# Kernel tuning notes

Measured on AMD Instinct MI355X. Metric: run time of the kernel, lower is better.

Reference implementation:

```python
import jax, jax.numpy as jnp
import numpy as np

R, B, F, H, C = 32, 2048, 512, 1024, 100  # n_rules, batch, n_fea, 2*n_fea, n_cls


def setup_inputs() -> dict:
    key = jax.random.key(0)
    ks = jax.random.split(key, 10)
    sc = lambda k, shape, fan: (jax.random.normal(k, shape, jnp.float32) / np.float32(np.sqrt(fan)))
    return {
        "data": jax.random.normal(ks[0], (B, F), jnp.float32),
        "proto": jax.random.normal(ks[1], (R, F), jnp.float32),
        "var": jax.random.uniform(ks[2], (R, F), jnp.float32, 0.5, 1.5),
        "fs_w1": sc(ks[3], (F, H), F), "fs_b1": jnp.zeros((H,), jnp.float32),
        "fs_w2": sc(ks[4], (H, F), H), "fs_b2": jnp.zeros((F,), jnp.float32),
        "fs_w3": sc(ks[5], (F, 1), F), "fs_b3": jnp.zeros((1,), jnp.float32),
        "cq_w1": sc(ks[6], (R, F, H), F), "cq_b1": jnp.zeros((R, H), jnp.float32),
        "cq_w2": sc(ks[7], (R, H, F), H), "cq_b2": jnp.zeros((R, F), jnp.float32),
        "cq_w3": sc(ks[8], (R, F, C), F), "cq_b3": jnp.zeros((R, C), jnp.float32),
        "is_train": 1,
    }


def reference(data, proto, var, fs_w1, fs_b1, fs_w2, fs_b2, fs_w3, fs_b3,
              cq_w1, cq_b1, cq_w2, cq_b2, cq_w3, cq_b3, is_train):
    # Gaussian fuzzy membership per rule: [R, B, F]
    fuzzy = jnp.exp(-(data[None, :, :] - proto[:, None, :]) ** 2
                    / (2.0 * var[:, None, :] ** 2))
    # shared fire-strength MLP applied per rule
    h = jax.nn.relu(jnp.einsum('rbf,fh->rbh', fuzzy, fs_w1) + fs_b1)
    h = jax.nn.relu(jnp.einsum('rbh,hf->rbf', h, fs_w2) + fs_b2)
    fs_logits = (jnp.einsum('rbf,fo->rbo', h, fs_w3) + fs_b3)[..., 0]  # [R, B]
    fire = jax.nn.softmax(fs_logits.T, axis=1)  # [B, R], softmax over rules
    # per-rule consequent MLPs on raw data (grouped GEMMs)
    g = jax.nn.relu(jnp.einsum('bf,rfh->rbh', data, cq_w1) + cq_b1[:, None, :])
    g = jax.nn.relu(jnp.einsum('rbh,rhf->rbf', g, cq_w2) + cq_b2[:, None, :])
    logits = jnp.einsum('rbf,rfc->rbc', g, cq_w3) + cq_b3[:, None, :]  # [R, B, C]
    # softmax-weighted expert sum, then class softmax
    out = jnp.einsum('br,rbc->bc', fire, logits)  # [B, C]
    return jax.nn.softmax(out, axis=1)
```

## Files before the change

kernel.cpp:

```cpp
#include <hip/hip_runtime.h>

typedef __attribute__((ext_vector_type(8))) short short8;
typedef __attribute__((ext_vector_type(4))) float f32x4;

__device__ __forceinline__ unsigned short f2bf(float f) {
    union { float f; unsigned u; } v; v.f = f;
    unsigned r = v.u + 0x7FFFu + ((v.u >> 16) & 1u);
    return (unsigned short)(r >> 16);
}
__device__ __forceinline__ float bf2f(unsigned short u) {
    union { unsigned u; float f; } v; v.u = ((unsigned)u) << 16;
    return v.f;
}

__global__ __launch_bounds__(256)
void cvt_bf16_kernel(const float* __restrict__ X, unsigned short* __restrict__ Y, int n4) {
    int i = blockIdx.x * 256 + threadIdx.x;
    if (i >= n4) return;
    float4 v = ((const float4*)X)[i];
    ushort4 o; o.x = f2bf(v.x); o.y = f2bf(v.y); o.z = f2bf(v.z); o.w = f2bf(v.w);
    ((ushort4*)Y)[i] = o;
}

__global__ __launch_bounds__(256)
void transpose_kernel(const float* __restrict__ X, unsigned short* __restrict__ Y,
                      int K, int N, int Np) {
    __shared__ float tile[32][33];
    int g = blockIdx.z;
    const float* Xg = X + (long)g * K * N;
    unsigned short* Yg = Y + (long)g * Np * K;
    int k0 = blockIdx.x * 32, n0 = blockIdx.y * 32;
    int tx = threadIdx.x & 31, ty = threadIdx.x >> 5;
#pragma unroll
    for (int i = 0; i < 4; ++i) {
        int kk = ty + i * 8;
        int n = n0 + tx;
        tile[kk][tx] = (n < N) ? Xg[(long)(k0 + kk) * N + n] : 0.0f;
    }
    __syncthreads();
#pragma unroll
    for (int i = 0; i < 4; ++i) {
        int nn = ty + i * 8;
        Yg[(long)(n0 + nn) * K + k0 + tx] = f2bf(tile[tx][nn]);
    }
}

__global__ __launch_bounds__(128)
void fuzzy_kernel(const float* __restrict__ data, const float* __restrict__ proto,
                  const float* __restrict__ var, unsigned short* __restrict__ fuzzy,
                  int r0) {
    int rb = blockIdx.x;
    int r = r0 + (rb >> 11), b = rb & 2047;
    int f = threadIdx.x * 4;
    float4 d = *(const float4*)(data + (long)b * 512 + f);
    float4 p = *(const float4*)(proto + (long)r * 512 + f);
    float4 w = *(const float4*)(var + (long)r * 512 + f);
    ushort4 o;
    float x;
    x = d.x - p.x; o.x = f2bf(__expf(-(x * x) / (2.f * w.x * w.x)));
    x = d.y - p.y; o.y = f2bf(__expf(-(x * x) / (2.f * w.y * w.y)));
    x = d.z - p.z; o.z = f2bf(__expf(-(x * x) / (2.f * w.z * w.z)));
    x = d.w - p.w; o.w = f2bf(__expf(-(x * x) / (2.f * w.w * w.w)));
    *(ushort4*)(fuzzy + (long)rb * 512 + f) = o;
}

#define RING_WAIT_BARRIER(n)                                        \
    asm volatile("s_waitcnt vmcnt(" #n ")" ::: "memory");           \
    __builtin_amdgcn_sched_barrier(0);                              \
    __builtin_amdgcn_s_barrier();                                   \
    __builtin_amdgcn_sched_barrier(0);

template<int EPI, bool RELU>
__global__ __launch_bounds__(512, 2)
void gemm256_kernel(const unsigned short* __restrict__ A,
                    const unsigned short* __restrict__ Bt,
                    const float* __restrict__ bias,
                    void* __restrict__ Cptr,
                    const float* __restrict__ w3,
                    float* __restrict__ fslog,
                    int nM, int nN, int K,
                    long sAg, long sBg, long sCg, int sBiasG) {
    unsigned tot = gridDim.x, bid = blockIdx.x;
    unsigned sw = (bid & 7u) * (tot >> 3) + (bid >> 3);
    unsigned pg = (unsigned)(nM * nN);
    unsigned g = sw / pg;
    unsigned rem = sw - g * pg;
    const int m0 = (int)(rem / (unsigned)nN) * 256;
    const int n0 = (int)(rem % (unsigned)nN) * 256;
    const int N = nN * 256;
    A += (long)g * sAg; Bt += (long)g * sBg; bias += (long)g * sBiasG;

    __shared__ __align__(16) unsigned short lds[8][8192];

    const int tid = threadIdx.x;
    const int lane = tid & 63;
    const int w = tid >> 6;
    const int wm = w >> 2, wn = w & 3;
    const int r16 = lane & 15, kg = lane >> 4;

    f32x4 acc[8][4];
#pragma unroll
    for (int i = 0; i < 8; ++i)
#pragma unroll
        for (int j = 0; j < 4; ++j) {
            f32x4 z = {0.f, 0.f, 0.f, 0.f};
            acc[i][j] = z;
        }

    const int nsteps = K >> 5;

    auto STAGE = [&](int slot, int kt) {
        const int k0 = kt << 5;
#pragma unroll
        for (int j = 0; j < 2; ++j) {
            int f = j * 512 + tid;
            int row = f >> 2, sl = f & 3;
            int kk = (sl ^ ((row >> 1) & 3)) << 3;
            const unsigned short* ga = A + (long)(m0 + row) * K + k0 + kk;
            __builtin_amdgcn_global_load_lds(
                (const __attribute__((address_space(1))) void*)ga,
                (__attribute__((address_space(3))) void*)(&lds[slot][0] + (j * 512 + w * 64) * 8),
                16, 0, 0);
            const unsigned short* gb = Bt + (long)(n0 + row) * K + k0 + kk;
            __builtin_amdgcn_global_load_lds(
                (const __attribute__((address_space(1))) void*)gb,
                (__attribute__((address_space(3))) void*)(&lds[4 + slot][0] + (j * 512 + w * 64) * 8),
                16, 0, 0);
        }
    };

    auto COMPUTE = [&](int slot) {
        short8 aF[8], bF[4];
#pragma unroll
        for (int mt = 0; mt < 8; ++mt) {
            int R = wm * 128 + mt * 16 + r16;
            aF[mt] = *(const short8*)(&lds[slot][0] + R * 32 + ((kg ^ ((R >> 1) & 3)) << 3));
        }
#pragma unroll
        for (int nt = 0; nt < 4; ++nt) {
            int R = wn * 64 + nt * 16 + r16;
            bF[nt] = *(const short8*)(&lds[4 + slot][0] + R * 32 + ((kg ^ ((R >> 1) & 3)) << 3));
        }
        __builtin_amdgcn_s_setprio(1);
#pragma unroll
        for (int mt = 0; mt < 8; ++mt)
#pragma unroll
            for (int nt = 0; nt < 4; ++nt)
                acc[mt][nt] = __builtin_amdgcn_mfma_f32_16x16x32_bf16(
                    aF[mt], bF[nt], acc[mt][nt], 0, 0, 0);
        __builtin_amdgcn_s_setprio(0);
        asm volatile("" ::: "memory");
        __builtin_amdgcn_s_barrier();
        __builtin_amdgcn_sched_barrier(0);
    };

    STAGE(0, 0); STAGE(1, 1); STAGE(2, 2);
    for (int t = 0; t <= nsteps - 3; ++t) {
        if (t + 3 < nsteps) STAGE((t + 3) & 3, t + 3);
        RING_WAIT_BARRIER(8);
        COMPUTE(t & 3);
    }
    { RING_WAIT_BARRIER(4); COMPUTE((nsteps - 2) & 3); }
    { RING_WAIT_BARRIER(0); COMPUTE((nsteps - 1) & 3); }

    if constexpr (EPI == 1) {
        float w3v[4], bv[4];
#pragma unroll
        for (int nt = 0; nt < 4; ++nt) {
            int col = n0 + wn * 64 + nt * 16 + r16;
            w3v[nt] = w3[col];
            bv[nt] = bias[col];
        }
#pragma unroll
        for (int mt = 0; mt < 8; ++mt) {
#pragma unroll
            for (int j = 0; j < 4; ++j) {
                float p = 0.f;
#pragma unroll
                for (int nt = 0; nt < 4; ++nt) {
                    float v = acc[mt][nt][j] + bv[nt];
                    if (RELU) v = fmaxf(v, 0.f);
                    p += v * w3v[nt];
                }
                p += __shfl_xor(p, 1, 64);
                p += __shfl_xor(p, 2, 64);
                p += __shfl_xor(p, 4, 64);
                p += __shfl_xor(p, 8, 64);
                if (r16 == 0) {
                    int row = m0 + wm * 128 + mt * 16 + kg * 4 + j;
                    atomicAdd(&fslog[row], p);
                }
            }
        }
    } else {
#pragma unroll
        for (int nt = 0; nt < 4; ++nt) {
            int col = n0 + wn * 64 + nt * 16 + r16;
            float bv = bias[col];
#pragma unroll
            for (int mt = 0; mt < 8; ++mt) {
#pragma unroll
                for (int j = 0; j < 4; ++j) {
                    int row = m0 + wm * 128 + mt * 16 + kg * 4 + j;
                    float v = acc[mt][nt][j] + bv;
                    if (RELU) v = fmaxf(v, 0.f);
                    ((unsigned short*)Cptr)[(long)g * sCg + (long)row * N + col] = f2bf(v);
                }
            }
        }
    }
}

template<int EPI, bool RELU>
__global__ __launch_bounds__(256, 2)
void gemm_kernel(const unsigned short* __restrict__ A,
                 const unsigned short* __restrict__ Bt,
                 const float* __restrict__ bias,
                 void* __restrict__ Cptr,
                 int nM, int nN, int K,
                 long sAg, long sBg, long sCg, int sBiasG, int biasN) {
    unsigned tot = gridDim.x;
    unsigned bid = blockIdx.x;
    unsigned sw = (tot & 7u) == 0 ? (bid & 7u) * (tot >> 3) + (bid >> 3) : bid;
    unsigned pg = (unsigned)nM * (unsigned)nN;
    unsigned g = sw / pg;
    unsigned rem = sw - g * pg;
    unsigned mt_ = rem / (unsigned)nN;
    unsigned nt_ = rem - mt_ * (unsigned)nN;
    const int N = nN * 128;
    A += (long)g * sAg;
    Bt += (long)g * sBg;
    bias += (long)g * sBiasG;
    const int m0 = (int)mt_ * 128;
    const int n0 = (int)nt_ * 128;

    __shared__ __align__(16) unsigned short ldsA[128 * 32];
    __shared__ __align__(16) unsigned short ldsB[128 * 32];

    const int tid = threadIdx.x;
    const int lane = tid & 63;
    const int w = tid >> 6;
    const int wm = w >> 1, wn = w & 1;
    const int r16 = lane & 15, kg = lane >> 4;

    f32x4 acc[4][4];
#pragma unroll
    for (int i = 0; i < 4; ++i)
#pragma unroll
        for (int j = 0; j < 4; ++j) {
            f32x4 z = {0.f, 0.f, 0.f, 0.f};
            acc[i][j] = z;
        }

    for (int k0 = 0; k0 < K; k0 += 32) {
#pragma unroll
        for (int j = 0; j < 2; ++j) {
            int t = j * 256 + tid;
            int row = t >> 2, kc = (t & 3) * 8;
            const unsigned short* ga = A + (long)(m0 + row) * K + k0 + kc;
            __builtin_amdgcn_global_load_lds(
                (const __attribute__((address_space(1))) void*)ga,
                (__attribute__((address_space(3))) void*)(ldsA + (j * 256 + w * 64) * 8),
                16, 0, 0);
            const unsigned short* gb = Bt + (long)(n0 + row) * K + k0 + kc;
            __builtin_amdgcn_global_load_lds(
                (const __attribute__((address_space(1))) void*)gb,
                (__attribute__((address_space(3))) void*)(ldsB + (j * 256 + w * 64) * 8),
                16, 0, 0);
        }
        __syncthreads();
        short8 aF[4], bF[4];
#pragma unroll
        for (int mt = 0; mt < 4; ++mt)
            aF[mt] = *(const short8*)(ldsA + (wm * 64 + mt * 16 + r16) * 32 + kg * 8);
#pragma unroll
        for (int nt = 0; nt < 4; ++nt)
            bF[nt] = *(const short8*)(ldsB + (wn * 64 + nt * 16 + r16) * 32 + kg * 8);
#pragma unroll
        for (int mt = 0; mt < 4; ++mt)
#pragma unroll
            for (int nt = 0; nt < 4; ++nt)
                acc[mt][nt] = __builtin_amdgcn_mfma_f32_16x16x32_bf16(
                    aF[mt], bF[nt], acc[mt][nt], 0, 0, 0);
        __syncthreads();
    }

#pragma unroll
    for (int nt = 0; nt < 4; ++nt) {
        int col = n0 + wn * 64 + nt * 16 + r16;
        float bv = (col < biasN) ? bias[col] : 0.f;
#pragma unroll
        for (int mt = 0; mt < 4; ++mt) {
#pragma unroll
            for (int j = 0; j < 4; ++j) {
                int row = m0 + wm * 64 + mt * 16 + kg * 4 + j;
                float v = acc[mt][nt][j] + bv;
                if (RELU) v = fmaxf(v, 0.f);
                if constexpr (EPI == 0)
                    ((unsigned short*)Cptr)[(long)g * sCg + (long)row * N + col] = f2bf(v);
                else
                    ((float*)Cptr)[(long)g * sCg + (long)row * N + col] = v;
            }
        }
    }
}

__global__ __launch_bounds__(256)
void fire_kernel(const float* __restrict__ fslog, float* __restrict__ fire) {
    int b = blockIdx.x * 256 + threadIdx.x;
    float v[32];
    float mx = -1e30f;
#pragma unroll
    for (int r = 0; r < 32; ++r) { v[r] = fslog[r * 2048 + b]; mx = fmaxf(mx, v[r]); }
    float s = 0.f;
#pragma unroll
    for (int r = 0; r < 32; ++r) { v[r] = __expf(v[r] - mx); s += v[r]; }
    float inv = 1.f / s;
#pragma unroll
    for (int r = 0; r < 32; ++r) fire[b * 32 + r] = v[r] * inv;
}

__global__ __launch_bounds__(128)
void accum_kernel(const float* __restrict__ logits, const float* __restrict__ fire,
                  float* __restrict__ mix, int r0, int NR, int first) {
    int b = blockIdx.x, c = threadIdx.x;
    float acc = first ? 0.f : mix[b * 128 + c];
    for (int r = 0; r < NR; ++r)
        acc += fire[b * 32 + r0 + r] * logits[((long)r * 2048 + b) * 128 + c];
    mix[b * 128 + c] = acc;
}

__global__ __launch_bounds__(128)
void softmax_out_kernel(const float* __restrict__ mix, float* __restrict__ out) {
    int b = blockIdx.x, c = threadIdx.x;
    __shared__ float redm[2], reds[2];
    float val = (c < 100) ? mix[b * 128 + c] : -1e30f;
    float m = val;
#pragma unroll
    for (int off = 32; off; off >>= 1) m = fmaxf(m, __shfl_xor(m, off, 64));
    int lane = c & 63, wv = c >> 6;
    if (lane == 0) redm[wv] = m;
    __syncthreads();
    m = fmaxf(redm[0], redm[1]);
    float e = (c < 100) ? __expf(val - m) : 0.f;
    float s = e;
#pragma unroll
    for (int off = 32; off; off >>= 1) s += __shfl_xor(s, off, 64);
    if (lane == 0) reds[wv] = s;
    __syncthreads();
    s = reds[0] + reds[1];
    if (c < 100) out[b * 100 + c] = e / s;
}

extern "C" void kernel_launch(void* const* d_in, const int* in_sizes, int n_in,
                              void* d_out, int out_size, void* d_ws, size_t ws_size,
                              hipStream_t stream) {
    const float* data  = (const float*)d_in[0];
    const float* proto = (const float*)d_in[1];
    const float* var   = (const float*)d_in[2];
    const float* fs_w1 = (const float*)d_in[3];
    const float* fs_b1 = (const float*)d_in[4];
    const float* fs_w2 = (const float*)d_in[5];
    const float* fs_b2 = (const float*)d_in[6];
    const float* fs_w3 = (const float*)d_in[7];
    const float* cq_w1 = (const float*)d_in[9];
    const float* cq_b1 = (const float*)d_in[10];
    const float* cq_w2 = (const float*)d_in[11];
    const float* cq_b2 = (const float*)d_in[12];
    const float* cq_w3 = (const float*)d_in[13];
    const float* cq_b3 = (const float*)d_in[14];
    float* out = (float*)d_out;

    const size_t PERSIST = 2097152 + 1048576 + 1048576 + 262144 + 262144 + 1048576;
    const size_t PER_RULE_P2 = 1048576 + 1048576 + 131072 + 2097152;
    auto need = [&](int p1r, int p2r) -> size_t {
        size_t logitsC = (size_t)p2r * 2048 * 128 * 4;
        size_t R0 = (size_t)p1r * 2048 * 512 * 2;
        size_t r0p2 = (size_t)p2r * PER_RULE_P2;
        if (r0p2 > R0) R0 = r0p2;
        size_t R1 = (size_t)p1r * 2048 * 1024 * 2;
        size_t g1b = (size_t)p2r * 2048 * 1024 * 2;
        if (g1b > R1) R1 = g1b;
        return PERSIST + logitsC + R0 + R1;
    };
    int p1r = 32, p2r = 16;
    while (need(p1r, p2r) > ws_size && p1r > 2) { p1r >>= 1; p2r >>= 1; }

    char* ws = (char*)d_ws;
    size_t off = 0;
    auto take = [&](size_t bytes) { char* p = ws + off; off += bytes; return p; };
    unsigned short* data_bf = (unsigned short*)take(2097152);
    unsigned short* w1t     = (unsigned short*)take(1048576);
    unsigned short* w2t     = (unsigned short*)take(1048576);
    float*          fslog   = (float*)take(262144);
    float*          fire    = (float*)take(262144);
    float*          mix     = (float*)take(1048576);
    float*          logitsC = (float*)take((size_t)p2r * 2048 * 128 * 4);
    size_t R0sz = (size_t)p1r * 2048 * 512 * 2;
    { size_t t = (size_t)p2r * PER_RULE_P2; if (t > R0sz) R0sz = t; }
    char* R0 = take(R0sz);
    size_t R1sz = (size_t)p1r * 2048 * 1024 * 2;
    { size_t t = (size_t)p2r * 2048 * 1024 * 2; if (t > R1sz) R1sz = t; }
    char* R1 = take(R1sz);

    unsigned short* cF   = (unsigned short*)R0;
    unsigned short* cW1t = (unsigned short*)R0;
    unsigned short* cW2t = (unsigned short*)(R0 + (size_t)p2r * 1048576);
    unsigned short* cW3t = (unsigned short*)(R0 + (size_t)p2r * 2097152);
    unsigned short* g2   = (unsigned short*)(R0 + (size_t)p2r * 2097152 + (size_t)p2r * 131072);
    unsigned short* h1   = (unsigned short*)R1;
    unsigned short* g1   = (unsigned short*)R1;

    cvt_bf16_kernel<<<1024, 256, 0, stream>>>(data, data_bf, 262144);
    transpose_kernel<<<dim3(16, 32, 1), 256, 0, stream>>>(fs_w1, w1t, 512, 1024, 1024);
    transpose_kernel<<<dim3(32, 16, 1), 256, 0, stream>>>(fs_w2, w2t, 1024, 512, 512);
    hipMemsetAsync(fslog, 0, 262144, stream);

    for (int ch = 0; ch < 32 / p1r; ++ch) {
        const int r0 = ch * p1r;
        fuzzy_kernel<<<p1r * 2048, 128, 0, stream>>>(data, proto, var, cF, r0);
        gemm256_kernel<0, true><<<p1r * 8 * 4, 512, 0, stream>>>(
            cF, w1t, fs_b1, h1, nullptr, nullptr,
            p1r * 8, 4, 512, 0, 0, 0, 0);
        gemm256_kernel<1, true><<<p1r * 8 * 2, 512, 0, stream>>>(
            h1, w2t, fs_b2, nullptr, fs_w3, fslog + (long)r0 * 2048,
            p1r * 8, 2, 1024, 0, 0, 0, 0);
    }
    fire_kernel<<<8, 256, 0, stream>>>(fslog, fire);

    for (int ch = 0; ch < 32 / p2r; ++ch) {
        const int r0 = ch * p2r;
        transpose_kernel<<<dim3(16, 32, p2r), 256, 0, stream>>>(
            cq_w1 + (long)r0 * 512 * 1024, cW1t, 512, 1024, 1024);
        transpose_kernel<<<dim3(32, 16, p2r), 256, 0, stream>>>(
            cq_w2 + (long)r0 * 1024 * 512, cW2t, 1024, 512, 512);
        transpose_kernel<<<dim3(16, 4, p2r), 256, 0, stream>>>(
            cq_w3 + (long)r0 * 512 * 100, cW3t, 512, 100, 128);
        gemm256_kernel<0, true><<<8 * 4 * p2r, 512, 0, stream>>>(
            data_bf, cW1t, cq_b1 + (long)r0 * 1024, g1, nullptr, nullptr,
            8, 4, 512, 0, (long)1024 * 512, (long)2048 * 1024, 1024);
        gemm256_kernel<0, true><<<8 * 2 * p2r, 512, 0, stream>>>(
            g1, cW2t, cq_b2 + (long)r0 * 512, g2, nullptr, nullptr,
            8, 2, 1024, (long)2048 * 1024, (long)512 * 1024, (long)2048 * 512, 512);
        gemm_kernel<2, false><<<16 * 1 * p2r, 256, 0, stream>>>(
            g2, cW3t, cq_b3 + (long)r0 * 100, logitsC,
            16, 1, 512, (long)2048 * 512, (long)128 * 512, (long)2048 * 128, 100, 100);
        accum_kernel<<<2048, 128, 0, stream>>>(logitsC, fire, mix, r0, p2r, ch == 0);
    }
    softmax_out_kernel<<<2048, 128, 0, stream>>>(mix, out);
}
```

Before: 536.7 us.

## Fuse fuzzy membership into first GEMM, fuse expert mixing into final GEMM

The Gaussian membership computation moves into the A-operand staging of a new first fire-strength GEMM, so the bf16 fuzzy tensor is never materialized. The reciprocal 1/(2·var²) is precomputed once. The per-rule logits GEMM now atomically accumulates fire-weighted outputs straight into the mix buffer, which removes the logits buffer and the accum kernel. The bf16 GEMM epilogue now stages through LDS to make 16-byte coalesced stores, and the rule chunking for phase one is removed by allocating the full h1 buffer. The costs are larger workspace, heavy float atomics on mix, and exp work sitting inside the GEMM main loop.

```diff
diff --git a/kernel.cpp b/kernel.cpp
--- a/kernel.cpp
+++ b/kernel.cpp
@@ -7,10 +7,6 @@
     union { float f; unsigned u; } v; v.f = f;
     unsigned r = v.u + 0x7FFFu + ((v.u >> 16) & 1u);
     return (unsigned short)(r >> 16);
-}
-__device__ __forceinline__ float bf2f(unsigned short u) {
-    union { unsigned u; float f; } v; v.u = ((unsigned)u) << 16;
-    return v.f;
 }
 
 __global__ __launch_bounds__(256)
@@ -20,6 +16,14 @@
     float4 v = ((const float4*)X)[i];
     ushort4 o; o.x = f2bf(v.x); o.y = f2bf(v.y); o.z = f2bf(v.z); o.w = f2bf(v.w);
     ((ushort4*)Y)[i] = o;
+}
+
+__global__ __launch_bounds__(256)
+void prep_var_kernel(const float* __restrict__ var, float* __restrict__ iv2, int n) {
+    int i = blockIdx.x * 256 + threadIdx.x;
+    if (i >= n) return;
+    float v = var[i];
+    iv2[i] = 1.f / (2.f * v * v);
 }
 
 __global__ __launch_bounds__(256)
@@ -43,25 +47,6 @@
         int nn = ty + i * 8;
         Yg[(long)(n0 + nn) * K + k0 + tx] = f2bf(tile[tx][nn]);
     }
-}
-
-__global__ __launch_bounds__(128)
-void fuzzy_kernel(const float* __restrict__ data, const float* __restrict__ proto,
-                  const float* __restrict__ var, unsigned short* __restrict__ fuzzy,
-                  int r0) {
-    int rb = blockIdx.x;
-    int r = r0 + (rb >> 11), b = rb & 2047;
-    int f = threadIdx.x * 4;
-    float4 d = *(const float4*)(data + (long)b * 512 + f);
-    float4 p = *(const float4*)(proto + (long)r * 512 + f);
-    float4 w = *(const float4*)(var + (long)r * 512 + f);
-    ushort4 o;
-    float x;
-    x = d.x - p.x; o.x = f2bf(__expf(-(x * x) / (2.f * w.x * w.x)));
-    x = d.y - p.y; o.y = f2bf(__expf(-(x * x) / (2.f * w.y * w.y)));
-    x = d.z - p.z; o.z = f2bf(__expf(-(x * x) / (2.f * w.z * w.z)));
-    x = d.w - p.w; o.w = f2bf(__expf(-(x * x) / (2.f * w.w * w.w)));
-    *(ushort4*)(fuzzy + (long)rb * 512 + f) = o;
 }
 
 #define RING_WAIT_BARRIER(n)                                        \
@@ -193,21 +178,174 @@
             }
         }
     } else {
-#pragma unroll
-        for (int nt = 0; nt < 4; ++nt) {
-            int col = n0 + wn * 64 + nt * 16 + r16;
-            float bv = bias[col];
-#pragma unroll
-            for (int mt = 0; mt < 8; ++mt) {
+        unsigned short* ldsC = &lds[0][0];
+        float bv[4];
+#pragma unroll
+        for (int nt = 0; nt < 4; ++nt) bv[nt] = bias[n0 + wn * 64 + nt * 16 + r16];
+#pragma unroll
+        for (int mt = 0; mt < 8; ++mt) {
+            int rr = wm * 128 + mt * 16 + kg * 4;
+#pragma unroll
+            for (int nt = 0; nt < 4; ++nt) {
+                int cc = wn * 64 + nt * 16 + r16;
 #pragma unroll
                 for (int j = 0; j < 4; ++j) {
-                    int row = m0 + wm * 128 + mt * 16 + kg * 4 + j;
-                    float v = acc[mt][nt][j] + bv;
+                    float v = acc[mt][nt][j] + bv[nt];
                     if (RELU) v = fmaxf(v, 0.f);
-                    ((unsigned short*)Cptr)[(long)g * sCg + (long)row * N + col] = f2bf(v);
+                    ldsC[(rr + j) * 256 + cc] = f2bf(v);
                 }
             }
         }
+        __syncthreads();
+        unsigned short* Cg = (unsigned short*)Cptr + (long)g * sCg;
+#pragma unroll
+        for (int rnd = 0; rnd < 16; ++rnd) {
+            int idx = rnd * 512 + tid;
+            int row = idx >> 5;
+            int c8 = idx & 31;
+            short8 vv = *(const short8*)(ldsC + row * 256 + c8 * 8);
+            *(short8*)(Cg + (long)(m0 + row) * N + n0 + c8 * 8) = vv;
+        }
+    }
+}
+
+__global__ __launch_bounds__(512, 2)
+void gemm_fs1_kernel(const float* __restrict__ data, const float* __restrict__ proto,
+                     const float* __restrict__ iv2, const unsigned short* __restrict__ Bt,
+                     const float* __restrict__ bias, unsigned short* __restrict__ C,
+                     int nM, int nN, int K) {
+    unsigned tot = gridDim.x, bid = blockIdx.x;
+    unsigned sw = (bid & 7u) * (tot >> 3) + (bid >> 3);
+    const int m0 = (int)(sw / (unsigned)nN) * 256;
+    const int n0 = (int)(sw % (unsigned)nN) * 256;
+    const int N = nN * 256;
+    const int r = m0 >> 11;
+    const int b0 = m0 & 2047;
+
+    __shared__ __align__(16) unsigned short lds[8][8192];
+
+    const int tid = threadIdx.x;
+    const int lane = tid & 63;
+    const int w = tid >> 6;
+    const int wm = w >> 2, wn = w & 3;
+    const int r16 = lane & 15, kg = lane >> 4;
+
+    f32x4 acc[8][4];
+#pragma unroll
+    for (int i = 0; i < 8; ++i)
+#pragma unroll
+        for (int j = 0; j < 4; ++j) {
+            f32x4 z = {0.f, 0.f, 0.f, 0.f};
+            acc[i][j] = z;
+        }
+
+    const int nsteps = K >> 5;
+    const int arow = tid >> 1;
+    const int kq = (tid & 1) * 16;
+
+    auto STAGE_B = [&](int bs, int kt) {
+        const int k0 = kt << 5;
+#pragma unroll
+        for (int j = 0; j < 2; ++j) {
+            int f = j * 512 + tid;
+            int row = f >> 2, sl = f & 3;
+            int kk = (sl ^ ((row >> 1) & 3)) << 3;
+            const unsigned short* gb = Bt + (long)(n0 + row) * K + k0 + kk;
+            __builtin_amdgcn_global_load_lds(
+                (const __attribute__((address_space(1))) void*)gb,
+                (__attribute__((address_space(3))) void*)(&lds[4 + bs][0] + (j * 512 + w * 64) * 8),
+                16, 0, 0);
+        }
+    };
+    auto LOADA = [&](float4* d, int kt) {
+        const float* src = data + (long)(b0 + arow) * 512 + (kt << 5) + kq;
+#pragma unroll
+        for (int q = 0; q < 4; ++q) d[q] = ((const float4*)src)[q];
+    };
+    auto WRITEA = [&](int as, int kt, const float4* d) {
+        const int k0 = (kt << 5) + kq;
+        const float* pp = proto + (long)r * 512 + k0;
+        const float* vv = iv2 + (long)r * 512 + k0;
+        short8 lo, hi;
+#pragma unroll
+        for (int q = 0; q < 4; ++q) {
+            float4 p = ((const float4*)pp)[q];
+            float4 iv = ((const float4*)vv)[q];
+            float x0 = d[q].x - p.x, x1 = d[q].y - p.y, x2 = d[q].z - p.z, x3 = d[q].w - p.w;
+            unsigned short e0 = f2bf(__expf(-(x0 * x0) * iv.x));
+            unsigned short e1 = f2bf(__expf(-(x1 * x1) * iv.y));
+            unsigned short e2 = f2bf(__expf(-(x2 * x2) * iv.z));
+            unsigned short e3 = f2bf(__expf(-(x3 * x3) * iv.w));
+            if (q < 2) { lo[q * 4] = (short)e0; lo[q * 4 + 1] = (short)e1; lo[q * 4 + 2] = (short)e2; lo[q * 4 + 3] = (short)e3; }
+            else { hi[(q - 2) * 4] = (short)e0; hi[(q - 2) * 4 + 1] = (short)e1; hi[(q - 2) * 4 + 2] = (short)e2; hi[(q - 2) * 4 + 3] = (short)e3; }
+        }
+        int rb2 = (arow >> 1) & 3;
+        int c0 = (kq >> 3) ^ rb2, c1 = ((kq >> 3) + 1) ^ rb2;
+        *(short8*)(&lds[as][0] + arow * 32 + c0 * 8) = lo;
+        *(short8*)(&lds[as][0] + arow * 32 + c1 * 8) = hi;
+    };
+    auto COMPUTE = [&](int slot) {
+        short8 aF[8], bF[4];
+#pragma unroll
+        for (int mt = 0; mt < 8; ++mt) {
+            int R = wm * 128 + mt * 16 + r16;
+            aF[mt] = *(const short8*)(&lds[slot][0] + R * 32 + ((kg ^ ((R >> 1) & 3)) << 3));
+        }
+#pragma unroll
+        for (int nt = 0; nt < 4; ++nt) {
+            int R = wn * 64 + nt * 16 + r16;
+            bF[nt] = *(const short8*)(&lds[4 + slot][0] + R * 32 + ((kg ^ ((R >> 1) & 3)) << 3));
+        }
+        __builtin_amdgcn_s_setprio(1);
+#pragma unroll
+        for (int mt = 0; mt < 8; ++mt)
+#pragma unroll
+            for (int nt = 0; nt < 4; ++nt)
+                acc[mt][nt] = __builtin_amdgcn_mfma_f32_16x16x32_bf16(
+                    aF[mt], bF[nt], acc[mt][nt], 0, 0, 0);
+        __builtin_amdgcn_s_setprio(0);
+    };
+
+    {
+        float4 d0[4];
+        LOADA(d0, 0);
+        STAGE_B(0, 0);
+        WRITEA(0, 0, d0);
+        __syncthreads();
+    }
+    for (int t = 0; t < nsteps; ++t) {
+        int s = t & 1;
+        float4 dn[4];
+        if (t + 1 < nsteps) { LOADA(dn, t + 1); STAGE_B(s ^ 1, t + 1); }
+        COMPUTE(s);
+        if (t + 1 < nsteps) WRITEA(s ^ 1, t + 1, dn);
+        __syncthreads();
+    }
+
+    unsigned short* ldsC = &lds[0][0];
+    float bv[4];
+#pragma unroll
+    for (int nt = 0; nt < 4; ++nt) bv[nt] = bias[n0 + wn * 64 + nt * 16 + r16];
+#pragma unroll
+    for (int mt = 0; mt < 8; ++mt) {
+        int rr = wm * 128 + mt * 16 + kg * 4;
+#pragma unroll
+        for (int nt = 0; nt < 4; ++nt) {
+            int cc = wn * 64 + nt * 16 + r16;
+#pragma unroll
+            for (int j = 0; j < 4; ++j) {
+                float v = fmaxf(acc[mt][nt][j] + bv[nt], 0.f);
+                ldsC[(rr + j) * 256 + cc] = f2bf(v);
+            }
+        }
+    }
+    __syncthreads();
+#pragma unroll
+    for (int rnd = 0; rnd < 16; ++rnd) {
+        int idx = rnd * 512 + tid;
+        int row = idx >> 5, c8 = idx & 31;
+        short8 vv = *(const short8*)(ldsC + row * 256 + c8 * 8);
+        *(short8*)(C + (long)(m0 + row) * N + n0 + c8 * 8) = vv;
     }
 }
 
@@ -218,7 +356,8 @@
                  const float* __restrict__ bias,
                  void* __restrict__ Cptr,
                  int nM, int nN, int K,
-                 long sAg, long sBg, long sCg, int sBiasG, int biasN) {
+                 long sAg, long sBg, long sCg, int sBiasG, int biasN,
+                 const float* __restrict__ fire, float* __restrict__ mix, int r0) {
     unsigned tot = gridDim.x;
     unsigned bid = blockIdx.x;
     unsigned sw = (tot & 7u) == 0 ? (bid & 7u) * (tot >> 3) + (bid >> 3) : bid;
@@ -285,21 +424,41 @@
         __syncthreads();
     }
 
-#pragma unroll
-    for (int nt = 0; nt < 4; ++nt) {
-        int col = n0 + wn * 64 + nt * 16 + r16;
-        float bv = (col < biasN) ? bias[col] : 0.f;
+    if constexpr (EPI == 3) {
+        float bv[4];
+#pragma unroll
+        for (int nt = 0; nt < 4; ++nt) {
+            int col = n0 + wn * 64 + nt * 16 + r16;
+            bv[nt] = (col < biasN) ? bias[col] : 0.f;
+        }
 #pragma unroll
         for (int mt = 0; mt < 4; ++mt) {
 #pragma unroll
             for (int j = 0; j < 4; ++j) {
                 int row = m0 + wm * 64 + mt * 16 + kg * 4 + j;
-                float v = acc[mt][nt][j] + bv;
-                if (RELU) v = fmaxf(v, 0.f);
-                if constexpr (EPI == 0)
-                    ((unsigned short*)Cptr)[(long)g * sCg + (long)row * N + col] = f2bf(v);
-                else
+                float f = fire[row * 32 + r0 + (int)g];
+#pragma unroll
+                for (int nt = 0; nt < 4; ++nt) {
+                    int col = n0 + wn * 64 + nt * 16 + r16;
+                    float v = acc[mt][nt][j] + bv[nt];
+                    atomicAdd(&mix[row * 128 + col], f * v);
+                }
+            }
+        }
+    } else {
+#pragma unroll
+        for (int nt = 0; nt < 4; ++nt) {
+            int col = n0 + wn * 64 + nt * 16 + r16;
+            float bv = (col < biasN) ? bias[col] : 0.f;
+#pragma unroll
+            for (int mt = 0; mt < 4; ++mt) {
+#pragma unroll
+                for (int j = 0; j < 4; ++j) {
+                    int row = m0 + wm * 64 + mt * 16 + kg * 4 + j;
+                    float v = acc[mt][nt][j] + bv;
+                    if (RELU) v = fmaxf(v, 0.f);
                     ((float*)Cptr)[(long)g * sCg + (long)row * N + col] = v;
+                }
             }
         }
     }
@@ -318,16 +477,6 @@
     float inv = 1.f / s;
 #pragma unroll
     for (int r = 0; r < 32; ++r) fire[b * 32 + r] = v[r] * inv;
-}
-
-__global__ __launch_bounds__(128)
-void accum_kernel(const float* __restrict__ logits, const float* __restrict__ fire,
-                  float* __restrict__ mix, int r0, int NR, int first) {
-    int b = blockIdx.x, c = threadIdx.x;
-    float acc = first ? 0.f : mix[b * 128 + c];
-    for (int r = 0; r < NR; ++r)
-        acc += fire[b * 32 + r0 + r] * logits[((long)r * 2048 + b) * 128 + c];
-    mix[b * 128 + c] = acc;
 }
 
 __global__ __launch_bounds__(128)
@@ -371,20 +520,14 @@
     const float* cq_b3 = (const float*)d_in[14];
     float* out = (float*)d_out;
 
-    const size_t PERSIST = 2097152 + 1048576 + 1048576 + 262144 + 262144 + 1048576;
-    const size_t PER_RULE_P2 = 1048576 + 1048576 + 131072 + 2097152;
-    auto need = [&](int p1r, int p2r) -> size_t {
-        size_t logitsC = (size_t)p2r * 2048 * 128 * 4;
-        size_t R0 = (size_t)p1r * 2048 * 512 * 2;
-        size_t r0p2 = (size_t)p2r * PER_RULE_P2;
-        if (r0p2 > R0) R0 = r0p2;
-        size_t R1 = (size_t)p1r * 2048 * 1024 * 2;
-        size_t g1b = (size_t)p2r * 2048 * 1024 * 2;
-        if (g1b > R1) R1 = g1b;
-        return PERSIST + logitsC + R0 + R1;
-    };
-    int p1r = 32, p2r = 16;
-    while (need(p1r, p2r) > ws_size && p1r > 2) { p1r >>= 1; p2r >>= 1; }
+    const size_t PERSIST = 2097152 + 1048576 + 1048576 + 65536 + 262144 + 262144 + 1048576;
+    const size_t H1SZ = (size_t)65536 * 1024 * 2;
+    auto need = [&](int p2r) -> size_t {
+        return PERSIST + H1SZ +
+               (size_t)p2r * (2048 * 512 * 2  + 1048576  + 1048576  + 131072 );
+    };
+    int p2r = 16;
+    while (need(p2r) > ws_size && p2r > 2) p2r >>= 1;
 
     char* ws = (char*)d_ws;
     size_t off = 0;
@@ -392,40 +535,28 @@
     unsigned short* data_bf = (unsigned short*)take(2097152);
     unsigned short* w1t     = (unsigned short*)take(1048576);
     unsigned short* w2t     = (unsigned short*)take(1048576);
+    float*          iv2     = (float*)take(65536);
     float*          fslog   = (float*)take(262144);
     float*          fire    = (float*)take(262144);
     float*          mix     = (float*)take(1048576);
-    float*          logitsC = (float*)take((size_t)p2r * 2048 * 128 * 4);
-    size_t R0sz = (size_t)p1r * 2048 * 512 * 2;
-    { size_t t = (size_t)p2r * PER_RULE_P2; if (t > R0sz) R0sz = t; }
-    char* R0 = take(R0sz);
-    size_t R1sz = (size_t)p1r * 2048 * 1024 * 2;
-    { size_t t = (size_t)p2r * 2048 * 1024 * 2; if (t > R1sz) R1sz = t; }
-    char* R1 = take(R1sz);
-
-    unsigned short* cF   = (unsigned short*)R0;
-    unsigned short* cW1t = (unsigned short*)R0;
-    unsigned short* cW2t = (unsigned short*)(R0 + (size_t)p2r * 1048576);
-    unsigned short* cW3t = (unsigned short*)(R0 + (size_t)p2r * 2097152);
-    unsigned short* g2   = (unsigned short*)(R0 + (size_t)p2r * 2097152 + (size_t)p2r * 131072);
-    unsigned short* h1   = (unsigned short*)R1;
-    unsigned short* g1   = (unsigned short*)R1;
+    unsigned short* h1      = (unsigned short*)take(H1SZ);
+    unsigned short* g2      = (unsigned short*)take((size_t)p2r * 2048 * 512 * 2);
+    unsigned short* cW1t    = (unsigned short*)take((size_t)p2r * 1048576);
+    unsigned short* cW2t    = (unsigned short*)take((size_t)p2r * 1048576);
+    unsigned short* cW3t    = (unsigned short*)take((size_t)p2r * 131072);
+    unsigned short* g1 = h1;
 
     cvt_bf16_kernel<<<1024, 256, 0, stream>>>(data, data_bf, 262144);
+    prep_var_kernel<<<64, 256, 0, stream>>>(var, iv2, 16384);
     transpose_kernel<<<dim3(16, 32, 1), 256, 0, stream>>>(fs_w1, w1t, 512, 1024, 1024);
     transpose_kernel<<<dim3(32, 16, 1), 256, 0, stream>>>(fs_w2, w2t, 1024, 512, 512);
     hipMemsetAsync(fslog, 0, 262144, stream);
-
-    for (int ch = 0; ch < 32 / p1r; ++ch) {
-        const int r0 = ch * p1r;
-        fuzzy_kernel<<<p1r * 2048, 128, 0, stream>>>(data, proto, var, cF, r0);
-        gemm256_kernel<0, true><<<p1r * 8 * 4, 512, 0, stream>>>(
-            cF, w1t, fs_b1, h1, nullptr, nullptr,
-            p1r * 8, 4, 512, 0, 0, 0, 0);
-        gemm256_kernel<1, true><<<p1r * 8 * 2, 512, 0, stream>>>(
-            h1, w2t, fs_b2, nullptr, fs_w3, fslog + (long)r0 * 2048,
-            p1r * 8, 2, 1024, 0, 0, 0, 0);
-    }
+    hipMemsetAsync(mix, 0, 1048576, stream);
+
+    gemm_fs1_kernel<<<256 * 4, 512, 0, stream>>>(
+        data, proto, iv2, w1t, fs_b1, h1, 256, 4, 512);
+    gemm256_kernel<1, true><<<256 * 2, 512, 0, stream>>>(
+        h1, w2t, fs_b2, nullptr, fs_w3, fslog, 256, 2, 1024, 0, 0, 0, 0);
     fire_kernel<<<8, 256, 0, stream>>>(fslog, fire);
 
     for (int ch = 0; ch < 32 / p2r; ++ch) {
@@ -442,10 +573,10 @@
         gemm256_kernel<0, true><<<8 * 2 * p2r, 512, 0, stream>>>(
             g1, cW2t, cq_b2 + (long)r0 * 512, g2, nullptr, nullptr,
             8, 2, 1024, (long)2048 * 1024, (long)512 * 1024, (long)2048 * 512, 512);
-        gemm_kernel<2, false><<<16 * 1 * p2r, 256, 0, stream>>>(
-            g2, cW3t, cq_b3 + (long)r0 * 100, logitsC,
-            16, 1, 512, (long)2048 * 512, (long)128 * 512, (long)2048 * 128, 100, 100);
-        accum_kernel<<<2048, 128, 0, stream>>>(logitsC, fire, mix, r0, p2r, ch == 0);
+        gemm_kernel<3, false><<<16 * 1 * p2r, 256, 0, stream>>>(
+            g2, cW3t, cq_b3 + (long)r0 * 100, nullptr,
+            16, 1, 512, (long)2048 * 512, (long)128 * 512, 0, 100, 100,
+            fire, mix, r0);
     }
     softmax_out_kernel<<<2048, 128, 0, stream>>>(mix, out);
 }
```

After: 548.9 us. 1.02x slower.

## Fuse expert accumulation into last GEMM, stage bf16 epilogue via LDS, unchunk fire path

Applied to the files above, without the earlier changes.

The separate accum kernel and the fp32 logits buffer are gone. The third consequent GEMM now multiplies its outputs by the fire weights and atomically adds them into a zeroed mix buffer. The bf16 store epilogue of the 256-tile GEMM now goes through LDS, so each thread writes coalesced 16-byte rows instead of scattered 2-byte stores. The fire-strength path always runs as one pass over all 32 rules, with a fixed-size workspace, instead of being chunked by workspace size. The cost is heavy float atomic contention on mix (32 rules per element) and a larger workspace requirement.

```diff
diff --git a/kernel.cpp b/kernel.cpp
--- a/kernel.cpp
+++ b/kernel.cpp
@@ -7,10 +7,6 @@
     union { float f; unsigned u; } v; v.f = f;
     unsigned r = v.u + 0x7FFFu + ((v.u >> 16) & 1u);
     return (unsigned short)(r >> 16);
-}
-__device__ __forceinline__ float bf2f(unsigned short u) {
-    union { unsigned u; float f; } v; v.u = ((unsigned)u) << 16;
-    return v.f;
 }
 
 __global__ __launch_bounds__(256)
@@ -47,10 +43,9 @@
 
 __global__ __launch_bounds__(128)
 void fuzzy_kernel(const float* __restrict__ data, const float* __restrict__ proto,
-                  const float* __restrict__ var, unsigned short* __restrict__ fuzzy,
-                  int r0) {
+                  const float* __restrict__ var, unsigned short* __restrict__ fuzzy) {
     int rb = blockIdx.x;
-    int r = r0 + (rb >> 11), b = rb & 2047;
+    int r = rb >> 11, b = rb & 2047;
     int f = threadIdx.x * 4;
     float4 d = *(const float4*)(data + (long)b * 512 + f);
     float4 p = *(const float4*)(proto + (long)r * 512 + f);
@@ -193,20 +188,33 @@
             }
         }
     } else {
-#pragma unroll
-        for (int nt = 0; nt < 4; ++nt) {
-            int col = n0 + wn * 64 + nt * 16 + r16;
-            float bv = bias[col];
-#pragma unroll
-            for (int mt = 0; mt < 8; ++mt) {
+        unsigned short* ldsC = &lds[0][0];
+        float bv[4];
+#pragma unroll
+        for (int nt = 0; nt < 4; ++nt) bv[nt] = bias[n0 + wn * 64 + nt * 16 + r16];
+#pragma unroll
+        for (int mt = 0; mt < 8; ++mt) {
+            int rr = wm * 128 + mt * 16 + kg * 4;
+#pragma unroll
+            for (int nt = 0; nt < 4; ++nt) {
+                int cc = wn * 64 + nt * 16 + r16;
 #pragma unroll
                 for (int j = 0; j < 4; ++j) {
-                    int row = m0 + wm * 128 + mt * 16 + kg * 4 + j;
-                    float v = acc[mt][nt][j] + bv;
+                    float v = acc[mt][nt][j] + bv[nt];
                     if (RELU) v = fmaxf(v, 0.f);
-                    ((unsigned short*)Cptr)[(long)g * sCg + (long)row * N + col] = f2bf(v);
+                    ldsC[(rr + j) * 256 + cc] = f2bf(v);
                 }
             }
+        }
+        __syncthreads();
+        unsigned short* Cg = (unsigned short*)Cptr + (long)g * sCg;
+#pragma unroll
+        for (int rnd = 0; rnd < 16; ++rnd) {
+            int idx = rnd * 512 + tid;
+            int row = idx >> 5;
+            int c8 = idx & 31;
+            short8 vv = *(const short8*)(ldsC + row * 256 + c8 * 8);
+            *(short8*)(Cg + (long)(m0 + row) * N + n0 + c8 * 8) = vv;
         }
     }
 }
@@ -218,7 +226,8 @@
                  const float* __restrict__ bias,
                  void* __restrict__ Cptr,
                  int nM, int nN, int K,
-                 long sAg, long sBg, long sCg, int sBiasG, int biasN) {
+                 long sAg, long sBg, long sCg, int sBiasG, int biasN,
+                 const float* __restrict__ fire, float* __restrict__ mix, int r0) {
     unsigned tot = gridDim.x;
     unsigned bid = blockIdx.x;
     unsigned sw = (tot & 7u) == 0 ? (bid & 7u) * (tot >> 3) + (bid >> 3) : bid;
@@ -285,21 +294,41 @@
         __syncthreads();
     }
 
-#pragma unroll
-    for (int nt = 0; nt < 4; ++nt) {
-        int col = n0 + wn * 64 + nt * 16 + r16;
-        float bv = (col < biasN) ? bias[col] : 0.f;
+    if constexpr (EPI == 3) {
+        float bv[4];
+#pragma unroll
+        for (int nt = 0; nt < 4; ++nt) {
+            int col = n0 + wn * 64 + nt * 16 + r16;
+            bv[nt] = (col < biasN) ? bias[col] : 0.f;
+        }
 #pragma unroll
         for (int mt = 0; mt < 4; ++mt) {
 #pragma unroll
             for (int j = 0; j < 4; ++j) {
                 int row = m0 + wm * 64 + mt * 16 + kg * 4 + j;
-                float v = acc[mt][nt][j] + bv;
-                if (RELU) v = fmaxf(v, 0.f);
-                if constexpr (EPI == 0)
-                    ((unsigned short*)Cptr)[(long)g * sCg + (long)row * N + col] = f2bf(v);
-                else
+                float f = fire[row * 32 + r0 + (int)g];
+#pragma unroll
+                for (int nt = 0; nt < 4; ++nt) {
+                    int col = n0 + wn * 64 + nt * 16 + r16;
+                    float v = acc[mt][nt][j] + bv[nt];
+                    atomicAdd(&mix[row * 128 + col], f * v);
+                }
+            }
+        }
+    } else {
+#pragma unroll
+        for (int nt = 0; nt < 4; ++nt) {
+            int col = n0 + wn * 64 + nt * 16 + r16;
+            float bv = (col < biasN) ? bias[col] : 0.f;
+#pragma unroll
+            for (int mt = 0; mt < 4; ++mt) {
+#pragma unroll
+                for (int j = 0; j < 4; ++j) {
+                    int row = m0 + wm * 64 + mt * 16 + kg * 4 + j;
+                    float v = acc[mt][nt][j] + bv;
+                    if (RELU) v = fmaxf(v, 0.f);
                     ((float*)Cptr)[(long)g * sCg + (long)row * N + col] = v;
+                }
             }
         }
     }
@@ -318,16 +347,6 @@
     float inv = 1.f / s;
 #pragma unroll
     for (int r = 0; r < 32; ++r) fire[b * 32 + r] = v[r] * inv;
-}
-
-__global__ __launch_bounds__(128)
-void accum_kernel(const float* __restrict__ logits, const float* __restrict__ fire,
-                  float* __restrict__ mix, int r0, int NR, int first) {
-    int b = blockIdx.x, c = threadIdx.x;
-    float acc = first ? 0.f : mix[b * 128 + c];
-    for (int r = 0; r < NR; ++r)
-        acc += fire[b * 32 + r0 + r] * logits[((long)r * 2048 + b) * 128 + c];
-    mix[b * 128 + c] = acc;
 }
 
 __global__ __launch_bounds__(128)
@@ -372,19 +391,14 @@
     float* out = (float*)d_out;
 
     const size_t PERSIST = 2097152 + 1048576 + 1048576 + 262144 + 262144 + 1048576;
-    const size_t PER_RULE_P2 = 1048576 + 1048576 + 131072 + 2097152;
-    auto need = [&](int p1r, int p2r) -> size_t {
-        size_t logitsC = (size_t)p2r * 2048 * 128 * 4;
-        size_t R0 = (size_t)p1r * 2048 * 512 * 2;
-        size_t r0p2 = (size_t)p2r * PER_RULE_P2;
-        if (r0p2 > R0) R0 = r0p2;
-        size_t R1 = (size_t)p1r * 2048 * 1024 * 2;
-        size_t g1b = (size_t)p2r * 2048 * 1024 * 2;
-        if (g1b > R1) R1 = g1b;
-        return PERSIST + logitsC + R0 + R1;
+    const size_t H1SZ = (size_t)65536 * 1024 * 2;
+    const size_t FUZZSZ = (size_t)65536 * 512 * 2;
+    auto need = [&](int p) -> size_t {
+        size_t fz = FUZZSZ > (size_t)p * 2097152 ? FUZZSZ : (size_t)p * 2097152;
+        return PERSIST + H1SZ + fz + (size_t)p * (1048576 + 1048576 + 131072);
     };
-    int p1r = 32, p2r = 16;
-    while (need(p1r, p2r) > ws_size && p1r > 2) { p1r >>= 1; p2r >>= 1; }
+    int p2r = 16;
+    while (need(p2r) > ws_size && p2r > 2) p2r >>= 1;
 
     char* ws = (char*)d_ws;
     size_t off = 0;
@@ -395,37 +409,26 @@
     float*          fslog   = (float*)take(262144);
     float*          fire    = (float*)take(262144);
     float*          mix     = (float*)take(1048576);
-    float*          logitsC = (float*)take((size_t)p2r * 2048 * 128 * 4);
-    size_t R0sz = (size_t)p1r * 2048 * 512 * 2;
-    { size_t t = (size_t)p2r * PER_RULE_P2; if (t > R0sz) R0sz = t; }
-    char* R0 = take(R0sz);
-    size_t R1sz = (size_t)p1r * 2048 * 1024 * 2;
-    { size_t t = (size_t)p2r * 2048 * 1024 * 2; if (t > R1sz) R1sz = t; }
-    char* R1 = take(R1sz);
-
-    unsigned short* cF   = (unsigned short*)R0;
-    unsigned short* cW1t = (unsigned short*)R0;
-    unsigned short* cW2t = (unsigned short*)(R0 + (size_t)p2r * 1048576);
-    unsigned short* cW3t = (unsigned short*)(R0 + (size_t)p2r * 2097152);
-    unsigned short* g2   = (unsigned short*)(R0 + (size_t)p2r * 2097152 + (size_t)p2r * 131072);
-    unsigned short* h1   = (unsigned short*)R1;
-    unsigned short* g1   = (unsigned short*)R1;
+    unsigned short* h1      = (unsigned short*)take(H1SZ);
+    size_t fzsz = FUZZSZ > (size_t)p2r * 2097152 ? FUZZSZ : (size_t)p2r * 2097152;
+    unsigned short* fuzzy   = (unsigned short*)take(fzsz);
+    unsigned short* cW1t    = (unsigned short*)take((size_t)p2r * 1048576);
+    unsigned short* cW2t    = (unsigned short*)take((size_t)p2r * 1048576);
+    unsigned short* cW3t    = (unsigned short*)take((size_t)p2r * 131072);
+    unsigned short* g1 = h1;
+    unsigned short* g2 = fuzzy;
 
     cvt_bf16_kernel<<<1024, 256, 0, stream>>>(data, data_bf, 262144);
     transpose_kernel<<<dim3(16, 32, 1), 256, 0, stream>>>(fs_w1, w1t, 512, 1024, 1024);
     transpose_kernel<<<dim3(32, 16, 1), 256, 0, stream>>>(fs_w2, w2t, 1024, 512, 512);
     hipMemsetAsync(fslog, 0, 262144, stream);
-
-    for (int ch = 0; ch < 32 / p1r; ++ch) {
-        const int r0 = ch * p1r;
-        fuzzy_kernel<<<p1r * 2048, 128, 0, stream>>>(data, proto, var, cF, r0);
-        gemm256_kernel<0, true><<<p1r * 8 * 4, 512, 0, stream>>>(
-            cF, w1t, fs_b1, h1, nullptr, nullptr,
-            p1r * 8, 4, 512, 0, 0, 0, 0);
-        gemm256_kernel<1, true><<<p1r * 8 * 2, 512, 0, stream>>>(
-            h1, w2t, fs_b2, nullptr, fs_w3, fslog + (long)r0 * 2048,
-            p1r * 8, 2, 1024, 0, 0, 0, 0);
-    }
+    hipMemsetAsync(mix, 0, 1048576, stream);
+
+    fuzzy_kernel<<<65536, 128, 0, stream>>>(data, proto, var, fuzzy);
+    gemm256_kernel<0, true><<<256 * 4, 512, 0, stream>>>(
+        fuzzy, w1t, fs_b1, h1, nullptr, nullptr, 256, 4, 512, 0, 0, 0, 0);
+    gemm256_kernel<1, true><<<256 * 2, 512, 0, stream>>>(
+        h1, w2t, fs_b2, nullptr, fs_w3, fslog, 256, 2, 1024, 0, 0, 0, 0);
     fire_kernel<<<8, 256, 0, stream>>>(fslog, fire);
 
     for (int ch = 0; ch < 32 / p2r; ++ch) {
@@ -442,10 +445,10 @@
         gemm256_kernel<0, true><<<8 * 2 * p2r, 512, 0, stream>>>(
             g1, cW2t, cq_b2 + (long)r0 * 512, g2, nullptr, nullptr,
             8, 2, 1024, (long)2048 * 1024, (long)512 * 1024, (long)2048 * 512, 512);
-        gemm_kernel<2, false><<<16 * 1 * p2r, 256, 0, stream>>>(
-            g2, cW3t, cq_b3 + (long)r0 * 100, logitsC,
-            16, 1, 512, (long)2048 * 512, (long)128 * 512, (long)2048 * 128, 100, 100);
-        accum_kernel<<<2048, 128, 0, stream>>>(logitsC, fire, mix, r0, p2r, ch == 0);
+        gemm_kernel<3, false><<<16 * 1 * p2r, 256, 0, stream>>>(
+            g2, cW3t, cq_b3 + (long)r0 * 100, nullptr,
+            16, 1, 512, (long)2048 * 512, (long)128 * 512, 0, 100, 100,
+            fire, mix, r0);
     }
     softmax_out_kernel<<<2048, 128, 0, stream>>>(mix, out);
 }
```

Result: faster. 522.5 us (-2.7%).
